# Kernel tuning notes

Measured on AMD Instinct MI355X. Metric: run time of the kernel, lower is better.

The kernel has to match this reference:

```python
import jax, jax.numpy as jnp
import numpy as np

K = 20
B, C_IN, N = 16, 3, 2048


def knn_idx(x, k):
    # x: [B, C, N] -> idx: [B, N, k] of nearest neighbors (incl. self)
    xt = jnp.swapaxes(x, 1, 2)                      # [B, N, C]
    inner = -2.0 * jnp.matmul(xt, x)                # [B, N, N]
    xx = jnp.sum(x * x, axis=1, keepdims=True)      # [B, 1, N]
    pd = -xx - inner - jnp.swapaxes(xx, 1, 2)       # negative sq. distance
    return jax.lax.top_k(pd, k)[1]                  # [B, N, k]


def graph_feature(x, k):
    # x: [B, C, N] -> edge features [B, 2C, N, k] = cat(nbr - ctr, ctr)
    idx = knn_idx(x, k)                             # [B, N, k]
    xt = jnp.swapaxes(x, 1, 2)                      # [B, N, C]
    nbr = jax.vmap(lambda pts, ids: pts[ids])(xt, idx)   # [B, N, k, C]
    ctr = jnp.broadcast_to(xt[:, :, None, :], nbr.shape)  # [B, N, k, C]
    feat = jnp.concatenate([nbr - ctr, ctr], axis=-1)     # [B, N, k, 2C]
    return jnp.transpose(feat, (0, 3, 1, 2))        # [B, 2C, N, k]


def conv2d_1x1(w, b, x):
    # w: [O, C], b: [O], x: [B, C, N, k]
    return jnp.einsum('oc,bcnk->bonk', w, x) + b[None, :, None, None]


def conv1d_1x1(w, b, x):
    # w: [O, C], b: [O], x: [B, C, N]
    return jnp.einsum('oc,bcn->bon', w, x) + b[None, :, None]


def setup_inputs() -> dict:
    key = jax.random.key(0)
    ks = jax.random.split(key, 13)
    def W(k, o, c):
        return jax.random.normal(k, (o, c), jnp.float32) * (1.0 / np.sqrt(c))
    x = jax.random.normal(ks[0], (B, C_IN, N), jnp.float32)
    return {
        'x': x,
        'w1': W(ks[1], 64, 6),    'b1': jnp.zeros((64,), jnp.float32),
        'w2': W(ks[2], 64, 64),   'b2': jnp.zeros((64,), jnp.float32),
        'w3': W(ks[3], 64, 128),  'b3': jnp.zeros((64,), jnp.float32),
        'w4': W(ks[4], 64, 64),   'b4': jnp.zeros((64,), jnp.float32),
        'w5': W(ks[5], 64, 128),  'b5': jnp.zeros((64,), jnp.float32),
        'w6': W(ks[6], 1024, 192),'b6': jnp.zeros((1024,), jnp.float32),
    }


def reference(x, w1, b1, w2, b2, w3, b3, w4, b4, w5, b5, w6, b6):
    # EdgeConv block 1
    f = graph_feature(x, K)                              # [B, 6, N, K]
    h = conv2d_1x1(w2, b2, conv2d_1x1(w1, b1, f))        # [B, 64, N, K]
    x1 = jnp.max(h, axis=-1)                             # [B, 64, N]
    # EdgeConv block 2
    f = graph_feature(x1, K)                             # [B, 128, N, K]
    h = conv2d_1x1(w4, b4, conv2d_1x1(w3, b3, f))
    x2 = jnp.max(h, axis=-1)                             # [B, 64, N]
    # EdgeConv block 3
    f = graph_feature(x2, K)                             # [B, 128, N, K]
    h = conv2d_1x1(w5, b5, f)
    x3 = jnp.max(h, axis=-1)                             # [B, 64, N]
    x123 = jnp.concatenate([x1, x2, x3], axis=1)         # [B, 192, N]
    x4 = conv1d_1x1(w6, b6, x123)                        # [B, 1024, N]
    x5 = jnp.max(x4, axis=-1)                            # [B, 1024] (adaptive max pool to 1)
    return (x123, x5[:, :, None])
```

## Files before the change

### kernel.cpp

```cpp
#include <hip/hip_runtime.h>

#define BB 16
#define NN 2048
#define KK 20

#define NEG_INF (-3.402823466e+38f)
#define DNEG (-1.0e300)

__global__ void prep_cmp(const float* __restrict__ w1, const float* __restrict__ b1,
                         const float* __restrict__ w2, const float* __restrict__ b2,
                         const float* __restrict__ w3, const float* __restrict__ b3,
                         const float* __restrict__ w4, const float* __restrict__ b4,
                         const float* __restrict__ w5, const float* __restrict__ b5,
                         double* __restrict__ wd2) {
    int t = threadIdx.x;
    for (int i = t; i < 192; i += 256) {
        int c = i >> 6, o = i & 63;
        double s = 0, sh = 0;
        for (int j = 0; j < 64; ++j) {
            double w2v = (double)w2[o * 64 + j];
            s  = fma(w2v, (double)w1[j * 6 + c], s);
            sh = fma(w2v, (double)w1[j * 6 + 3 + c], sh);
        }
        wd2[i] = s;
        wd2[192 + i] = sh - s;
    }
    for (int i = t; i < 64; i += 256) {
        double s = (double)b2[i];
        for (int j = 0; j < 64; ++j)
            s = fma((double)w2[i * 64 + j], (double)b1[j], s);
        wd2[384 + i] = s;
        double s2 = (double)b4[i];
        for (int j = 0; j < 64; ++j)
            s2 = fma((double)w4[i * 64 + j], (double)b3[j], s2);
        wd2[8640 + i] = s2;
        wd2[16896 + i] = (double)b5[i];
    }
    for (int i = t; i < 4096; i += 256) {
        int c = i >> 6, o = i & 63;
        double s = 0, sh = 0;
        for (int j = 0; j < 64; ++j) {
            double w4v = (double)w4[o * 64 + j];
            s  = fma(w4v, (double)w3[j * 128 + c], s);
            sh = fma(w4v, (double)w3[j * 128 + 64 + c], sh);
        }
        wd2[448 + i] = s;
        wd2[4544 + i] = sh - s;
        double lo = (double)w5[o * 128 + c];
        wd2[8704 + i] = lo;
        wd2[12800 + i] = (double)w5[o * 128 + 64 + c] - lo;
    }
}

__device__ __forceinline__ unsigned long long pkey(float v, int col) {
    float vc = __fadd_rn(v, 0.0f);
    unsigned u = __float_as_uint(vc);
    unsigned s = (unsigned)((int)u >> 31);
    unsigned m = u ^ (s | 0x80000000u);
    return ((unsigned long long)m << 32) | (unsigned)(2047 - col);
}

__device__ __forceinline__ void top2k_upd(unsigned long long k,
        unsigned long long& ka, unsigned long long& kb) {
    bool gta = k > ka;
    bool gtb = k > kb;
    unsigned long long nkb = gta ? ka : (gtb ? k : kb);
    ka = gta ? k : ka;
    kb = nkb;
}

__device__ __forceinline__ void topk20_key(float* vrow, int lane,
        unsigned long long ka, unsigned long long kb, int* outp) {
    int myout = 0;
    #pragma unroll 1
    for (int it = 0; it < 20; ++it) {
        unsigned long long wk = ka;
        #pragma unroll
        for (int d = 32; d; d >>= 1) {
            unsigned long long o = __shfl_xor(wk, d);
            wk = (o > wk) ? o : wk;
        }
        int widx = 2047 - (int)(wk & 0xFFFFFFFFull);
        if (lane == it) myout = widx;
        if (ka == wk) {
            vrow[widx] = NEG_INF;
            ka = kb;
            kb = 0ULL;
        }
        if (ka == 0ULL) {
            kb = 0ULL;
            #pragma unroll 1
            for (int s = 0; s < 8; ++s) {
                int base = s * 256 + lane * 4;
                float4 v4 = *(const float4*)&vrow[base];
                top2k_upd(pkey(v4.x, base + 0), ka, kb);
                top2k_upd(pkey(v4.y, base + 1), ka, kb);
                top2k_upd(pkey(v4.z, base + 2), ka, kb);
                top2k_upd(pkey(v4.w, base + 3), ka, kb);
            }
        }
    }
    if (lane < 20) outp[lane] = myout;
}

__global__ void norms1_k(const float* __restrict__ x, float* __restrict__ nrm) {
    int t = blockIdx.x * 256 + threadIdx.x;
    int b = t >> 11, n = t & 2047;
    const float* xb = x + (size_t)b * 3 * NN;
    float cx = xb[n], cy = xb[NN + n], cz = xb[2 * NN + n];
    nrm[t] = __fadd_rn(__fadd_rn(__fmul_rn(cx, cx), __fmul_rn(cy, cy)),
                       __fmul_rn(cz, cz));
}

__global__ void knn1_k(const float* __restrict__ x, const float* __restrict__ nrm,
                       int* __restrict__ idx) {
    __shared__ float vlds[2][2048];
    int lane = threadIdx.x & 63, w = threadIdx.x >> 6;
    int b = blockIdx.y, r = blockIdx.x * 2 + w;
    const float* xb = x + (size_t)b * 3 * NN;
    const float* nb_ = nrm + (size_t)b * NN;
    float rx = xb[r], ry = xb[NN + r], rz = xb[2 * NN + r];
    float xxi = nb_[r];
    float* vrow = vlds[w];
    unsigned long long ka = 0ULL, kb = 0ULL;
    #pragma unroll 1
    for (int s = 0; s < 8; ++s) {
        int base = s * 256 + lane * 4;
        float4 cx = *(const float4*)&xb[base];
        float4 cy = *(const float4*)&xb[NN + base];
        float4 cz = *(const float4*)&xb[2 * NN + base];
        float4 xx4 = *(const float4*)&nb_[base];
        float4 nd4;
        {
            float dot = fmaf(rz, cz.x, fmaf(ry, cy.x, __fmul_rn(rx, cx.x)));
            float inner = __fmul_rn(-2.f, dot);
            float t1 = __fsub_rn(-xx4.x, inner);
            nd4.x = __fsub_rn(t1, xxi);
        }
        {
            float dot = fmaf(rz, cz.y, fmaf(ry, cy.y, __fmul_rn(rx, cx.y)));
            float inner = __fmul_rn(-2.f, dot);
            float t1 = __fsub_rn(-xx4.y, inner);
            nd4.y = __fsub_rn(t1, xxi);
        }
        {
            float dot = fmaf(rz, cz.z, fmaf(ry, cy.z, __fmul_rn(rx, cx.z)));
            float inner = __fmul_rn(-2.f, dot);
            float t1 = __fsub_rn(-xx4.z, inner);
            nd4.z = __fsub_rn(t1, xxi);
        }
        {
            float dot = fmaf(rz, cz.w, fmaf(ry, cy.w, __fmul_rn(rx, cx.w)));
            float inner = __fmul_rn(-2.f, dot);
            float t1 = __fsub_rn(-xx4.w, inner);
            nd4.w = __fsub_rn(t1, xxi);
        }
        *(float4*)&vrow[base] = nd4;
        top2k_upd(pkey(nd4.x, base + 0), ka, kb);
        top2k_upd(pkey(nd4.y, base + 1), ka, kb);
        top2k_upd(pkey(nd4.z, base + 2), ka, kb);
        top2k_upd(pkey(nd4.w, base + 3), ka, kb);
    }
    topk20_key(vrow, lane, ka, kb, idx + ((size_t)b * NN + r) * KK);
}

__global__ void norms23_k(const float* __restrict__ x123t, int coff,
                          float* __restrict__ nrm) {
    int t = blockIdx.x * 256 + threadIdx.x;
    const float* r = x123t + (size_t)t * 192 + coff;
    float acc = 0.f;
    #pragma unroll 1
    for (int c = 0; c < 64; c += 4) {
        float4 q = *(const float4*)(r + c);
        acc = __fadd_rn(acc, __fmul_rn(q.x, q.x));
        acc = __fadd_rn(acc, __fmul_rn(q.y, q.y));
        acc = __fadd_rn(acc, __fmul_rn(q.z, q.z));
        acc = __fadd_rn(acc, __fmul_rn(q.w, q.w));
    }
    nrm[t] = acc;
}

__global__ __launch_bounds__(256) void gemm_pd_k(const float* __restrict__ dout,
        int coff, const float* __restrict__ nrm, float* __restrict__ pd, int b0) {
    __shared__ float As[64][68];
    __shared__ float Bs[64][68];
    int b = b0 + blockIdx.z;
    int rb = blockIdx.y * 64, cb = blockIdx.x * 64;
    const float* doutc = dout + (size_t)(b * 192 + coff) * NN;
    int tid = threadIdx.x;
    int cq = tid >> 4, qd = (tid & 15) * 4;
    #pragma unroll
    for (int cc = 0; cc < 64; cc += 16) {
        float4 a = *(const float4*)(doutc + (size_t)(cc + cq) * NN + rb + qd);
        As[cc + cq][qd + 0] = a.x; As[cc + cq][qd + 1] = a.y;
        As[cc + cq][qd + 2] = a.z; As[cc + cq][qd + 3] = a.w;
        float4 bv = *(const float4*)(doutc + (size_t)(cc + cq) * NN + cb + qd);
        Bs[cc + cq][qd + 0] = bv.x; Bs[cc + cq][qd + 1] = bv.y;
        Bs[cc + cq][qd + 2] = bv.z; Bs[cc + cq][qd + 3] = bv.w;
    }
    __syncthreads();
    int tx = tid & 15, ty = tid >> 4;
    float acc[4][4];
    #pragma unroll
    for (int i = 0; i < 4; ++i)
        #pragma unroll
        for (int j = 0; j < 4; ++j) acc[i][j] = 0.f;
    #pragma unroll 4
    for (int c = 0; c < 64; ++c) {
        float4 av4 = *(const float4*)&As[c][ty * 4];
        float4 bv4 = *(const float4*)&Bs[c][tx * 4];
        float aa[4] = {av4.x, av4.y, av4.z, av4.w};
        float bb[4] = {bv4.x, bv4.y, bv4.z, bv4.w};
        #pragma unroll
        for (int i = 0; i < 4; ++i)
            #pragma unroll
            for (int j = 0; j < 4; ++j)
                acc[i][j] = fmaf(aa[i], bb[j], acc[i][j]);
    }
    const float* nb_ = nrm + (size_t)b * NN;
    #pragma unroll
    for (int i = 0; i < 4; ++i) {
        int r = rb + ty * 4 + i;
        float xxi = nb_[r];
        float4 o4;
        float* o = (float*)&o4;
        #pragma unroll
        for (int j = 0; j < 4; ++j) {
            float xxj = nb_[cb + tx * 4 + j];
            float inner = __fmul_rn(-2.f, acc[i][j]);
            float t1 = __fsub_rn(-xxj, inner);
            o[j] = __fsub_rn(t1, xxi);
        }
        *(float4*)(pd + ((size_t)blockIdx.z * NN + r) * NN + cb + tx * 4) = o4;
    }
}

__global__ void select_k(const float* __restrict__ pd, int* __restrict__ idx, int b0) {
    __shared__ float vlds[4][2048];
    int lane = threadIdx.x & 63, w = threadIdx.x >> 6;
    int bb = blockIdx.y, r = blockIdx.x * 4 + w;
    const float* row = pd + ((size_t)bb * NN + r) * NN;
    float* vrow = vlds[w];
    unsigned long long ka = 0ULL, kb = 0ULL;
    #pragma unroll 1
    for (int s = 0; s < 8; ++s) {
        int base = s * 256 + lane * 4;
        float4 v4 = *(const float4*)&row[base];
        *(float4*)&vrow[base] = v4;
        top2k_upd(pkey(v4.x, base + 0), ka, kb);
        top2k_upd(pkey(v4.y, base + 1), ka, kb);
        top2k_upd(pkey(v4.z, base + 2), ka, kb);
        top2k_upd(pkey(v4.w, base + 3), ka, kb);
    }
    topk20_key(vrow, lane, ka, kb, idx + ((size_t)(b0 + bb) * NN + r) * KK);
}

__global__ __launch_bounds__(256) void ab1_k(const float* __restrict__ x,
        const double* __restrict__ wd2, double* __restrict__ Ad,
        double* __restrict__ Bd) {
    int tid = threadIdx.x, lane = tid & 63, w = tid >> 6;
    int p = blockIdx.x * 4 + w, b = p >> 11, n = p & 2047;
    const float* xb = x + (size_t)b * 3 * NN;
    double c0 = (double)xb[n], c1 = (double)xb[NN + n], c2 = (double)xb[2 * NN + n];
    double A = wd2[384 + lane];
    A = fma(wd2[192 + 0 * 64 + lane], c0, A);
    A = fma(wd2[192 + 1 * 64 + lane], c1, A);
    A = fma(wd2[192 + 2 * 64 + lane], c2, A);
    double B = wd2[0 * 64 + lane] * c0;
    B = fma(wd2[1 * 64 + lane], c1, B);
    B = fma(wd2[2 * 64 + lane], c2, B);
    Ad[(size_t)p * 64 + lane] = A;
    Bd[(size_t)p * 64 + lane] = B;
}

__global__ __launch_bounds__(256) void ab23_k(const float* __restrict__ x123t,
        const double* __restrict__ wd2, int coff, int woffW, int woffWd, int goff,
        double* __restrict__ Ad, double* __restrict__ Bd) {
    __shared__ double Ws[4096];
    __shared__ double ctr[4][64];
    int tid = threadIdx.x, lane = tid & 63, w = tid >> 6;
    for (int i = tid; i < 4096; i += 256) Ws[i] = wd2[woffW + i];
    __syncthreads();
    int p0 = blockIdx.x * 64 + w * 16;
    #pragma unroll 1
    for (int it = 0; it < 16; ++it) {
        int p = p0 + it, b = p >> 11, n = p & 2047;
        ctr[w][lane] = (double)x123t[((size_t)b * NN + n) * 192 + coff + lane];
        double a0 = wd2[goff + lane], a1 = 0, a2 = 0, a3 = 0;
        double q0 = 0, q1 = 0, q2 = 0, q3 = 0;
        #pragma unroll
        for (int c = 0; c < 64; c += 4) {
            double x0 = ctr[w][c + 0], x1 = ctr[w][c + 1];
            double x2 = ctr[w][c + 2], x3 = ctr[w][c + 3];
            a0 = fma(wd2[woffWd + (c + 0) * 64 + lane], x0, a0);
            a1 = fma(wd2[woffWd + (c + 1) * 64 + lane], x1, a1);
            a2 = fma(wd2[woffWd + (c + 2) * 64 + lane], x2, a2);
            a3 = fma(wd2[woffWd + (c + 3) * 64 + lane], x3, a3);
            q0 = fma(Ws[(c + 0) * 64 + lane], x0, q0);
            q1 = fma(Ws[(c + 1) * 64 + lane], x1, q1);
            q2 = fma(Ws[(c + 2) * 64 + lane], x2, q2);
            q3 = fma(Ws[(c + 3) * 64 + lane], x3, q3);
        }
        Ad[(size_t)p * 64 + lane] = (a0 + a1) + (a2 + a3);
        Bd[(size_t)p * 64 + lane] = (q0 + q1) + (q2 + q3);
    }
}

__global__ __launch_bounds__(256) void gmax_k(const double* __restrict__ Ad,
        const double* __restrict__ Bd, const int* __restrict__ idxb, int cho,
        float* __restrict__ dout, float* __restrict__ x123t_o) {
    int tid = threadIdx.x, lane = tid & 63, w = tid >> 6;
    int p = blockIdx.x * 4 + w, b = p >> 11, n = p & 2047;
    const int* ip = idxb + (size_t)p * KK;
    size_t boff = (size_t)(b << 11);
    double m = DNEG;
    int nbc = ip[0];
    double v = Bd[(boff + nbc) * 64 + lane];
    #pragma unroll 1
    for (int kk = 0; kk < KK; ++kk) {
        double cur = v;
        if (kk < KK - 1) {
            int nbn = ip[kk + 1];
            v = Bd[(boff + nbn) * 64 + lane];
        }
        m = fmax(m, cur);
    }
    double out = Ad[(size_t)p * 64 + lane] + m;
    dout[((size_t)b * 192 + cho + lane) * NN + n] = (float)out;
    x123t_o[((size_t)b * NN + n) * 192 + cho + lane] = (float)out;
}

#define KC 32
__global__ __launch_bounds__(256) void w6_k(const float* __restrict__ x123t,
                                            const float* __restrict__ w6,
                                            float* __restrict__ partial6) {
    __shared__ float xs[KC][136];
    __shared__ float wsb[KC][68];
    __shared__ float red[64][17];
    int tid = threadIdx.x;
    int ntile = blockIdx.x & 15, ot = (blockIdx.x >> 4) & 15, b = blockIdx.x >> 8;
    int n0 = ntile * 128, o0 = ot * 64;
    int ln2 = tid >> 1, lc2 = (tid & 1) * 16;
    int lw = tid >> 2, lcw = (tid & 3) * 8;
    const float* xrow = x123t + ((size_t)b * NN + n0 + ln2) * 192 + lc2;
    const float* wrow = w6 + (size_t)(o0 + lw) * 192 + lcw;
    float acc[4][8];
    #pragma unroll
    for (int i = 0; i < 4; ++i)
        #pragma unroll
        for (int j = 0; j < 8; ++j) acc[i][j] = 0.f;
    int to = tid & 15, tn = tid >> 4;
    for (int cc = 0; cc < 192; cc += KC) {
        float4 xa = *(const float4*)(xrow + cc);
        float4 xb4 = *(const float4*)(xrow + cc + 4);
        float4 xc4 = *(const float4*)(xrow + cc + 8);
        float4 xd4 = *(const float4*)(xrow + cc + 12);
        float4 wa = *(const float4*)(wrow + cc);
        float4 wb4 = *(const float4*)(wrow + cc + 4);
        __syncthreads();
        {
            float v[16] = {xa.x, xa.y, xa.z, xa.w, xb4.x, xb4.y, xb4.z, xb4.w,
                           xc4.x, xc4.y, xc4.z, xc4.w, xd4.x, xd4.y, xd4.z, xd4.w};
            #pragma unroll
            for (int q = 0; q < 16; ++q) {
                int row = lc2 + q;
                xs[row][ln2 ^ (row & 24)] = v[q];
            }
        }
        {
            float v[8] = {wa.x, wa.y, wa.z, wa.w, wb4.x, wb4.y, wb4.z, wb4.w};
            #pragma unroll
            for (int q = 0; q < 8; ++q) {
                int row = lcw + q;
                wsb[row][lw ^ (row & 24)] = v[q];
            }
        }
        __syncthreads();
        #pragma unroll
        for (int k = 0; k < KC; ++k) {
            int kx = k & 24;
            float4 wv = *(const float4*)&wsb[k][(to * 4) ^ kx];
            float4 xv1 = *(const float4*)&xs[k][(tn * 8) ^ kx];
            float4 xv2 = *(const float4*)&xs[k][((tn * 8) ^ kx) + 4];
            float wr[4] = {wv.x, wv.y, wv.z, wv.w};
            float xr[8] = {xv1.x, xv1.y, xv1.z, xv1.w,
                           xv2.x, xv2.y, xv2.z, xv2.w};
            #pragma unroll
            for (int i = 0; i < 4; ++i)
                #pragma unroll
                for (int j = 0; j < 8; ++j)
                    acc[i][j] = fmaf(wr[i], xr[j], acc[i][j]);
        }
    }
    #pragma unroll
    for (int i = 0; i < 4; ++i) {
        float m0 = fmaxf(fmaxf(acc[i][0], acc[i][1]), fmaxf(acc[i][2], acc[i][3]));
        float m1 = fmaxf(fmaxf(acc[i][4], acc[i][5]), fmaxf(acc[i][6], acc[i][7]));
        red[to * 4 + i][tn] = fmaxf(m0, m1);
    }
    __syncthreads();
    if (tid < 64) {
        float mm = red[tid][0];
        #pragma unroll
        for (int t = 1; t < 16; ++t) mm = fmaxf(mm, red[tid][t]);
        partial6[((size_t)b * 1024 + o0 + tid) * 16 + ntile] = mm;
    }
}

__global__ void final_k(const float* __restrict__ partial6, const float* __restrict__ b6,
                        float* __restrict__ dout) {
    int t = blockIdx.x * 256 + threadIdx.x;
    int o = t & 1023;
    float m = NEG_INF;
    #pragma unroll 1
    for (int nt = 0; nt < 16; ++nt) m = fmaxf(m, partial6[(size_t)t * 16 + nt]);
    dout[(size_t)BB * 192 * NN + t] = m + b6[o];
}

extern "C" void kernel_launch(void* const* d_in, const int* in_sizes, int n_in,
                              void* d_out_, int out_size, void* d_ws, size_t ws_size,
                              hipStream_t stream) {
    (void)in_sizes; (void)n_in; (void)out_size;
    const float* x  = (const float*)d_in[0];
    const float* w1 = (const float*)d_in[1];
    const float* b1 = (const float*)d_in[2];
    const float* w2 = (const float*)d_in[3];
    const float* b2 = (const float*)d_in[4];
    const float* w3 = (const float*)d_in[5];
    const float* b3 = (const float*)d_in[6];
    const float* w4 = (const float*)d_in[7];
    const float* b4 = (const float*)d_in[8];
    const float* w5 = (const float*)d_in[9];
    const float* b5 = (const float*)d_in[10];
    const float* w6 = (const float*)d_in[11];
    const float* b6 = (const float*)d_in[12];
    float* dout = (float*)d_out_;

    char* ws = (char*)d_ws;
    float*  x123t    = (float*)(ws + 0);
    int*    idxb     = (int*)(ws + 25165824);
    float*  nrm      = (float*)(ws + 27787264);
    float*  partial6 = (float*)(ws + 27918336);
    double* wd2      = (double*)(ws + 30015488);
    char*   region   = ws + 30151168;
    float*  pd = (float*)region;
    double* Ad = (double*)region;
    double* Bd = (double*)(region + 16777216);
    long long avail = (long long)ws_size - 30151168LL;
    int nb = (int)(avail / 16777216LL);
    if (nb < 2) nb = 2;
    if (nb > 8) nb = 8;

    prep_cmp<<<1, 256, 0, stream>>>(w1, b1, w2, b2, w3, b3, w4, b4, w5, b5, wd2);

    norms1_k<<<128, 256, 0, stream>>>(x, nrm);
    knn1_k<<<dim3(1024, BB), 128, 0, stream>>>(x, nrm, idxb);
    ab1_k<<<8192, 256, 0, stream>>>(x, wd2, Ad, Bd);
    gmax_k<<<8192, 256, 0, stream>>>(Ad, Bd, idxb, 0, dout, x123t);

    norms23_k<<<128, 256, 0, stream>>>(x123t, 0, nrm);
    for (int b0 = 0; b0 < BB; b0 += nb) {
        int cur = (BB - b0 < nb) ? (BB - b0) : nb;
        gemm_pd_k<<<dim3(32, 32, cur), 256, 0, stream>>>(dout, 0, nrm, pd, b0);
        select_k<<<dim3(512, cur), 256, 0, stream>>>(pd, idxb, b0);
    }
    ab23_k<<<512, 256, 0, stream>>>(x123t, wd2, 0, 448, 4544, 8640, Ad, Bd);
    gmax_k<<<8192, 256, 0, stream>>>(Ad, Bd, idxb, 64, dout, x123t);

    norms23_k<<<128, 256, 0, stream>>>(x123t, 64, nrm);
    for (int b0 = 0; b0 < BB; b0 += nb) {
        int cur = (BB - b0 < nb) ? (BB - b0) : nb;
        gemm_pd_k<<<dim3(32, 32, cur), 256, 0, stream>>>(dout, 64, nrm, pd, b0);
        select_k<<<dim3(512, cur), 256, 0, stream>>>(pd, idxb, b0);
    }
    ab23_k<<<512, 256, 0, stream>>>(x123t, wd2, 64, 8704, 12800, 16896, Ad, Bd);
    gmax_k<<<8192, 256, 0, stream>>>(Ad, Bd, idxb, 128, dout, x123t);

    w6_k<<<4096, 256, 0, stream>>>(x123t, w6, partial6);
    final_k<<<64, 256, 0, stream>>>(partial6, b6, dout);
}
```

Before: 1.250 ms.

## Drop LDS row copies in top-k selection; rescan source with key threshold

The kNN selection kernels no longer stage each distance row in shared memory or mark taken entries with -inf. When a lane runs out of its top-2 candidates, it rescans the original source (the pd row in global memory, or recomputed distances for block 1) and keeps only keys below the last extracted winner. This frees LDS so more waves fit per CU, and knn1 now runs 4 rows per 256-thread block. The cost is extra global reads or distance recomputation on each refill.

```diff
diff --git a/kernel.cpp b/kernel.cpp
--- a/kernel.cpp
+++ b/kernel.cpp
@@ -69,40 +69,6 @@
     kb = nkb;
 }
 
-__device__ __forceinline__ void topk20_key(float* vrow, int lane,
-        unsigned long long ka, unsigned long long kb, int* outp) {
-    int myout = 0;
-    #pragma unroll 1
-    for (int it = 0; it < 20; ++it) {
-        unsigned long long wk = ka;
-        #pragma unroll
-        for (int d = 32; d; d >>= 1) {
-            unsigned long long o = __shfl_xor(wk, d);
-            wk = (o > wk) ? o : wk;
-        }
-        int widx = 2047 - (int)(wk & 0xFFFFFFFFull);
-        if (lane == it) myout = widx;
-        if (ka == wk) {
-            vrow[widx] = NEG_INF;
-            ka = kb;
-            kb = 0ULL;
-        }
-        if (ka == 0ULL) {
-            kb = 0ULL;
-            #pragma unroll 1
-            for (int s = 0; s < 8; ++s) {
-                int base = s * 256 + lane * 4;
-                float4 v4 = *(const float4*)&vrow[base];
-                top2k_upd(pkey(v4.x, base + 0), ka, kb);
-                top2k_upd(pkey(v4.y, base + 1), ka, kb);
-                top2k_upd(pkey(v4.z, base + 2), ka, kb);
-                top2k_upd(pkey(v4.w, base + 3), ka, kb);
-            }
-        }
-    }
-    if (lane < 20) outp[lane] = myout;
-}
-
 __global__ void norms1_k(const float* __restrict__ x, float* __restrict__ nrm) {
     int t = blockIdx.x * 256 + threadIdx.x;
     int b = t >> 11, n = t & 2047;
@@ -112,16 +78,14 @@
                        __fmul_rn(cz, cz));
 }
 
-__global__ void knn1_k(const float* __restrict__ x, const float* __restrict__ nrm,
-                       int* __restrict__ idx) {
-    __shared__ float vlds[2][2048];
+__global__ __launch_bounds__(256) void knn1_k(const float* __restrict__ x,
+        const float* __restrict__ nrm, int* __restrict__ idx) {
     int lane = threadIdx.x & 63, w = threadIdx.x >> 6;
-    int b = blockIdx.y, r = blockIdx.x * 2 + w;
+    int b = blockIdx.y, r = blockIdx.x * 4 + w;
     const float* xb = x + (size_t)b * 3 * NN;
     const float* nb_ = nrm + (size_t)b * NN;
     float rx = xb[r], ry = xb[NN + r], rz = xb[2 * NN + r];
     float xxi = nb_[r];
-    float* vrow = vlds[w];
     unsigned long long ka = 0ULL, kb = 0ULL;
     #pragma unroll 1
     for (int s = 0; s < 8; ++s) {
@@ -130,38 +94,83 @@
         float4 cy = *(const float4*)&xb[NN + base];
         float4 cz = *(const float4*)&xb[2 * NN + base];
         float4 xx4 = *(const float4*)&nb_[base];
-        float4 nd4;
         {
             float dot = fmaf(rz, cz.x, fmaf(ry, cy.x, __fmul_rn(rx, cx.x)));
             float inner = __fmul_rn(-2.f, dot);
             float t1 = __fsub_rn(-xx4.x, inner);
-            nd4.x = __fsub_rn(t1, xxi);
+            top2k_upd(pkey(__fsub_rn(t1, xxi), base + 0), ka, kb);
         }
         {
             float dot = fmaf(rz, cz.y, fmaf(ry, cy.y, __fmul_rn(rx, cx.y)));
             float inner = __fmul_rn(-2.f, dot);
             float t1 = __fsub_rn(-xx4.y, inner);
-            nd4.y = __fsub_rn(t1, xxi);
+            top2k_upd(pkey(__fsub_rn(t1, xxi), base + 1), ka, kb);
         }
         {
             float dot = fmaf(rz, cz.z, fmaf(ry, cy.z, __fmul_rn(rx, cx.z)));
             float inner = __fmul_rn(-2.f, dot);
             float t1 = __fsub_rn(-xx4.z, inner);
-            nd4.z = __fsub_rn(t1, xxi);
+            top2k_upd(pkey(__fsub_rn(t1, xxi), base + 2), ka, kb);
         }
         {
             float dot = fmaf(rz, cz.w, fmaf(ry, cy.w, __fmul_rn(rx, cx.w)));
             float inner = __fmul_rn(-2.f, dot);
             float t1 = __fsub_rn(-xx4.w, inner);
-            nd4.w = __fsub_rn(t1, xxi);
-        }
-        *(float4*)&vrow[base] = nd4;
-        top2k_upd(pkey(nd4.x, base + 0), ka, kb);
-        top2k_upd(pkey(nd4.y, base + 1), ka, kb);
-        top2k_upd(pkey(nd4.z, base + 2), ka, kb);
-        top2k_upd(pkey(nd4.w, base + 3), ka, kb);
-    }
-    topk20_key(vrow, lane, ka, kb, idx + ((size_t)b * NN + r) * KK);
+            top2k_upd(pkey(__fsub_rn(t1, xxi), base + 3), ka, kb);
+        }
+    }
+    int myout = 0;
+    #pragma unroll 1
+    for (int it = 0; it < 20; ++it) {
+        unsigned long long wk = ka;
+        #pragma unroll
+        for (int d = 32; d; d >>= 1) {
+            unsigned long long o = __shfl_xor(wk, d);
+            wk = (o > wk) ? o : wk;
+        }
+        if (lane == it) myout = 2047 - (int)(wk & 0xFFFFFFFFull);
+        if (ka == wk) { ka = kb; kb = 0ULL; }
+        if (ka == 0ULL) {
+            kb = 0ULL;
+            #pragma unroll 1
+            for (int s = 0; s < 8; ++s) {
+                int base = s * 256 + lane * 4;
+                float4 cx = *(const float4*)&xb[base];
+                float4 cy = *(const float4*)&xb[NN + base];
+                float4 cz = *(const float4*)&xb[2 * NN + base];
+                float4 xx4 = *(const float4*)&nb_[base];
+                {
+                    float dot = fmaf(rz, cz.x, fmaf(ry, cy.x, __fmul_rn(rx, cx.x)));
+                    float inner = __fmul_rn(-2.f, dot);
+                    float t1 = __fsub_rn(-xx4.x, inner);
+                    unsigned long long k = pkey(__fsub_rn(t1, xxi), base + 0);
+                    if (k < wk) top2k_upd(k, ka, kb);
+                }
+                {
+                    float dot = fmaf(rz, cz.y, fmaf(ry, cy.y, __fmul_rn(rx, cx.y)));
+                    float inner = __fmul_rn(-2.f, dot);
+                    float t1 = __fsub_rn(-xx4.y, inner);
+                    unsigned long long k = pkey(__fsub_rn(t1, xxi), base + 1);
+                    if (k < wk) top2k_upd(k, ka, kb);
+                }
+                {
+                    float dot = fmaf(rz, cz.z, fmaf(ry, cy.z, __fmul_rn(rx, cx.z)));
+                    float inner = __fmul_rn(-2.f, dot);
+                    float t1 = __fsub_rn(-xx4.z, inner);
+                    unsigned long long k = pkey(__fsub_rn(t1, xxi), base + 2);
+                    if (k < wk) top2k_upd(k, ka, kb);
+                }
+                {
+                    float dot = fmaf(rz, cz.w, fmaf(ry, cy.w, __fmul_rn(rx, cx.w)));
+                    float inner = __fmul_rn(-2.f, dot);
+                    float t1 = __fsub_rn(-xx4.w, inner);
+                    unsigned long long k = pkey(__fsub_rn(t1, xxi), base + 3);
+                    if (k < wk) top2k_upd(k, ka, kb);
+                }
+            }
+        }
+    }
+    if (lane < 20) idx[((size_t)b * NN + r) * KK + lane] = myout;
 }
 
 __global__ void norms23_k(const float* __restrict__ x123t, int coff,
@@ -235,24 +244,50 @@
     }
 }
 
-__global__ void select_k(const float* __restrict__ pd, int* __restrict__ idx, int b0) {
-    __shared__ float vlds[4][2048];
+__global__ __launch_bounds__(256) void select_k(const float* __restrict__ pd,
+        int* __restrict__ idx, int b0) {
     int lane = threadIdx.x & 63, w = threadIdx.x >> 6;
     int bb = blockIdx.y, r = blockIdx.x * 4 + w;
     const float* row = pd + ((size_t)bb * NN + r) * NN;
-    float* vrow = vlds[w];
     unsigned long long ka = 0ULL, kb = 0ULL;
     #pragma unroll 1
     for (int s = 0; s < 8; ++s) {
         int base = s * 256 + lane * 4;
         float4 v4 = *(const float4*)&row[base];
-        *(float4*)&vrow[base] = v4;
         top2k_upd(pkey(v4.x, base + 0), ka, kb);
         top2k_upd(pkey(v4.y, base + 1), ka, kb);
         top2k_upd(pkey(v4.z, base + 2), ka, kb);
         top2k_upd(pkey(v4.w, base + 3), ka, kb);
     }
-    topk20_key(vrow, lane, ka, kb, idx + ((size_t)(b0 + bb) * NN + r) * KK);
+    int myout = 0;
+    #pragma unroll 1
+    for (int it = 0; it < 20; ++it) {
+        unsigned long long wk = ka;
+        #pragma unroll
+        for (int d = 32; d; d >>= 1) {
+            unsigned long long o = __shfl_xor(wk, d);
+            wk = (o > wk) ? o : wk;
+        }
+        if (lane == it) myout = 2047 - (int)(wk & 0xFFFFFFFFull);
+        if (ka == wk) { ka = kb; kb = 0ULL; }
+        if (ka == 0ULL) {
+            kb = 0ULL;
+            #pragma unroll 1
+            for (int s = 0; s < 8; ++s) {
+                int base = s * 256 + lane * 4;
+                float4 v4 = *(const float4*)&row[base];
+                unsigned long long k0 = pkey(v4.x, base + 0);
+                if (k0 < wk) top2k_upd(k0, ka, kb);
+                unsigned long long k1 = pkey(v4.y, base + 1);
+                if (k1 < wk) top2k_upd(k1, ka, kb);
+                unsigned long long k2 = pkey(v4.z, base + 2);
+                if (k2 < wk) top2k_upd(k2, ka, kb);
+                unsigned long long k3 = pkey(v4.w, base + 3);
+                if (k3 < wk) top2k_upd(k3, ka, kb);
+            }
+        }
+    }
+    if (lane < 20) idx[((size_t)(b0 + bb) * NN + r) * KK + lane] = myout;
 }
 
 __global__ __launch_bounds__(256) void ab1_k(const float* __restrict__ x,
@@ -454,7 +489,7 @@
     prep_cmp<<<1, 256, 0, stream>>>(w1, b1, w2, b2, w3, b3, w4, b4, w5, b5, wd2);
 
     norms1_k<<<128, 256, 0, stream>>>(x, nrm);
-    knn1_k<<<dim3(1024, BB), 128, 0, stream>>>(x, nrm, idxb);
+    knn1_k<<<dim3(512, BB), 256, 0, stream>>>(x, nrm, idxb);
     ab1_k<<<8192, 256, 0, stream>>>(x, wd2, Ad, Bd);
     gmax_k<<<8192, 256, 0, stream>>>(Ad, Bd, idxb, 0, dout, x123t);
 
```

Result: no change. 1.234 ms (-1.3%).
